# Optimization experiments

Measured on AMD Instinct MI355X. Metric: run time of the kernel, lower is better.

The kernel has to match this reference:

```python
import jax, jax.numpy as jnp
import numpy as np

N = 100000   # nodes
E = 800000   # edges
IN = 128     # input feature dim
H = 2        # heads
C = 64       # hidden_dim (per-head channels)
OUT = 40     # classes
L = 3        # num_layers
EPS = 1e-16  # matches torch_geometric.utils.softmax denominator eps


def setup_inputs() -> dict:
    key = jax.random.key(0)
    ks = jax.random.split(key, 4 * L + 6)
    inp = {}
    inp["x"] = jax.random.normal(ks[0], (N, IN), dtype=jnp.float32)
    inp["edge_index"] = jax.random.randint(ks[1], (2, E), 0, N, dtype=jnp.int32)
    dims = [IN] + [H * C] * (L - 1)
    ki = 2
    for l in range(L):
        d = dims[l]
        inp[f"W{l}"] = jax.random.normal(ks[ki], (H * C, d), dtype=jnp.float32) / np.float32(np.sqrt(d)); ki += 1
        inp[f"b{l}"] = jnp.zeros((H * C,), dtype=jnp.float32)
        inp[f"al{l}"] = jax.random.normal(ks[ki], (H, C), dtype=jnp.float32) * 0.1; ki += 1
        inp[f"ar{l}"] = jax.random.normal(ks[ki], (H, C), dtype=jnp.float32) * 0.1; ki += 1
    inp["Wp1"] = jax.random.normal(ks[ki], (C, H * C), dtype=jnp.float32) / np.float32(np.sqrt(H * C)); ki += 1
    inp["bp1"] = jnp.zeros((C,), dtype=jnp.float32)
    inp["Wp2"] = jax.random.normal(ks[ki], (OUT, C), dtype=jnp.float32) / np.float32(np.sqrt(C)); ki += 1
    inp["bp2"] = jnp.zeros((OUT,), dtype=jnp.float32)
    return inp


def _gat_layer(x, W, b, al, ar, src, dst):
    # lin_l == lin_r (shared weights in the original)
    h = (x @ W.T + b).reshape(-1, H, C)          # [N, H, C]
    alpha_l = al * h                              # source-side scores [N, H, C]
    alpha_r = ar * h                              # target-side scores [N, H, C]
    # per-edge raw attention logits; NOTE: original computes leaky_relu(alpha)
    # but then applies softmax to the RAW sum (faithful to source code).
    e = alpha_r[dst] + alpha_l[src]               # [E, H, C]
    m = jax.ops.segment_max(e, dst, num_segments=N)
    w = jnp.exp(e - m[dst])
    s = jax.ops.segment_sum(w, dst, num_segments=N)
    att = w / (s[dst] + EPS)                      # segment softmax per target node
    out = jax.ops.segment_sum(att * h[src], dst, num_segments=N)  # [N, H, C]
    return out.reshape(-1, H * C)


def reference(x, edge_index, W0, b0, al0, ar0, W1, b1, al1, ar1, W2, b2, al2, ar2,
              Wp1, bp1, Wp2, bp2):
    src, dst = edge_index[0], edge_index[1]
    layers = [(W0, b0, al0, ar0), (W1, b1, al1, ar1), (W2, b2, al2, ar2)]
    h = x
    for (W, b, al, ar) in layers:
        h = _gat_layer(h, W, b, al, ar, src, dst)
        h = jax.nn.relu(h)  # dropout p=0 -> identity
    h = h @ Wp1.T + bp1
    h = h @ Wp2.T + bp2
    return jax.nn.log_softmax(h, axis=1)
```

## Files before the change

kernel.cpp:

```cpp
#include <hip/hip_runtime.h>
#include <hip/hip_bf16.h>
#include <math.h>

#define NN 100000
#define EE 800000
#define DD 128
#define OUTC 40

constexpr int NBUCK = (NN + 511) >> 9;
constexpr int BCAP  = 6144;
constexpr int EB    = 8192;

typedef short bf16x8 __attribute__((ext_vector_type(8)));
typedef float f32x4 __attribute__((ext_vector_type(4)));

__device__ __forceinline__ ushort f2bf(float f) {
  unsigned u = __float_as_uint(f);
  u = (u + 0x7FFFu + ((u >> 16) & 1u)) >> 16;
  return (ushort)u;
}
__device__ __forceinline__ float bflo(unsigned u) { return __uint_as_float(u << 16); }
__device__ __forceinline__ float bfhi(unsigned u) { return __uint_as_float(u & 0xFFFF0000u); }

__device__ __forceinline__ int swz(int row, int kbyte) {
  return row * 256 + (kbyte ^ ((row & 7) << 4));
}

__global__ __launch_bounds__(256) void k_initcur(int* __restrict__ cursor0) {
  int b = threadIdx.x;
  if (b < NBUCK) cursor0[b] = b * BCAP;
}

__global__ __launch_bounds__(256) void k_binA(const int* __restrict__ src, const int* __restrict__ dst,
                                              int* __restrict__ cursor0, int2* __restrict__ binned, int e) {
  __shared__ int cnt[NBUCK], base[NBUCK], cnt2[NBUCK];
  int t = threadIdx.x;
  for (int b = t; b < NBUCK; b += 256) { cnt[b] = 0; cnt2[b] = 0; }
  __syncthreads();
  int e0 = blockIdx.x * EB;
#pragma unroll
  for (int p = 0; p < EB / 256; ++p) {
    int i = e0 + p * 256 + t;
    if (i < e) atomicAdd(&cnt[dst[i] >> 9], 1);
  }
  __syncthreads();
  for (int b = t; b < NBUCK; b += 256)
    if (cnt[b] > 0) base[b] = atomicAdd(&cursor0[b], cnt[b]);
  __syncthreads();
#pragma unroll
  for (int p = 0; p < EB / 256; ++p) {
    int i = e0 + p * 256 + t;
    if (i < e) {
      int d = dst[i];
      int bk = d >> 9;
      int pos = base[bk] + atomicAdd(&cnt2[bk], 1);
      binned[pos] = make_int2(src[i], d);
    }
  }
}

__global__ __launch_bounds__(256) void k_degB(const int* __restrict__ cursor0,
                                              const int2* __restrict__ binned,
                                              int* __restrict__ deg, int n) {
  __shared__ int cnt[512];
  int b = blockIdx.x, t = threadIdx.x;
  cnt[t] = 0; cnt[t + 256] = 0;
  __syncthreads();
  int node0 = b << 9;
  int beg = b * BCAP;
  int cend = cursor0[b];
  for (int i = beg + t; i < cend; i += 256)
    atomicAdd(&cnt[binned[i].y - node0], 1);
  __syncthreads();
  if (node0 + t < n) deg[node0 + t] = cnt[t];
  if (node0 + t + 256 < n) deg[node0 + t + 256] = cnt[t + 256];
}

__global__ __launch_bounds__(1024) void k_scan1(const int* __restrict__ deg, int* __restrict__ rp,
                                                int* __restrict__ bsum, int n) {
  __shared__ int s[1024];
  int t = threadIdx.x;
  int i = blockIdx.x * 1024 + t;
  s[t] = (i < n) ? deg[i] : 0;
  __syncthreads();
  for (int off = 1; off < 1024; off <<= 1) {
    int x = (t >= off) ? s[t - off] : 0;
    __syncthreads();
    s[t] += x;
    __syncthreads();
  }
  if (i < n) rp[i + 1] = s[t];
  if (t == 1023) bsum[blockIdx.x] = s[1023];
}

__global__ __launch_bounds__(128) void k_scan2(int* __restrict__ bsum, int nb) {
  __shared__ int s[128];
  int t = threadIdx.x;
  s[t] = (t < nb) ? bsum[t] : 0;
  __syncthreads();
  for (int off = 1; off < 128; off <<= 1) {
    int x = (t >= off) ? s[t - off] : 0;
    __syncthreads();
    s[t] += x;
    __syncthreads();
  }
  if (t < nb) bsum[t] = s[t];
}

__global__ void k_scan3(int* __restrict__ rp, const int* __restrict__ bsum, int n) {
  int i = blockIdx.x * 256 + threadIdx.x;
  if (i == 0) rp[0] = 0;
  if (i < n) {
    int blk = i >> 10;
    rp[i + 1] = rp[i + 1] + ((blk > 0) ? bsum[blk - 1] : 0);
  }
}

__global__ __launch_bounds__(256) void k_scatC(const int* __restrict__ cursor0,
                                               const int2* __restrict__ binned,
                                               const int* __restrict__ rp,
                                               int* __restrict__ col, int n) {
  __shared__ int cur[512];
  __shared__ int lrp[512];
  int b = blockIdx.x, t = threadIdx.x;
  cur[t] = 0; cur[t + 256] = 0;
  int node0 = b << 9;
  lrp[t] = (node0 + t < n) ? rp[node0 + t] : 0;
  lrp[t + 256] = (node0 + t + 256 < n) ? rp[node0 + t + 256] : 0;
  __syncthreads();
  int beg = b * BCAP;
  int cend = cursor0[b];
  for (int i = beg + t; i < cend; i += 256) {
    int2 p = binned[i];
    int d = p.y - node0;
    int pos = lrp[d] + atomicAdd(&cur[d], 1);
    col[pos] = p.x;
  }
}

template<bool INF32>
__global__ __launch_bounds__(256, 2) void k_mfma_gemm(const void* __restrict__ xin,
                                                      const float* __restrict__ W,
                                                      const float* __restrict__ bias,
                                                      ushort* __restrict__ outp, int n) {
  __shared__ __align__(16) char lds[65536];
  const int t = threadIdx.x;
  const int node0 = blockIdx.x * 128;

  if (INF32) {
#pragma unroll
    for (int p = 0; p < 16; ++p) {
      int F = p * 256 + t;
      int r = F >> 5, cchunk = F & 31;
      int node = node0 + r;
      float4 v = make_float4(0.f, 0.f, 0.f, 0.f);
      if (node < n) v = *(const float4*)((const float*)xin + (size_t)node * DD + cchunk * 4);
      ushort q[4] = {f2bf(v.x), f2bf(v.y), f2bf(v.z), f2bf(v.w)};
      *(unsigned long long*)(lds + swz(r, cchunk * 8)) = *(unsigned long long*)q;
    }
  } else {
#pragma unroll
    for (int p = 0; p < 8; ++p) {
      int F = p * 256 + t;
      int r = F >> 4, cchunk = F & 15;
      int node = node0 + r;
      uint4 v = make_uint4(0u, 0u, 0u, 0u);
      if (node < n) v = *(const uint4*)((const ushort*)xin + (size_t)node * DD + cchunk * 8);
      *(uint4*)(lds + swz(r, cchunk * 16)) = v;
    }
  }
  {
#pragma unroll
    for (int p = 0; p < 16; ++p) {
      int F = p * 256 + t;
      int r = F >> 5, cchunk = F & 31;
      float4 v = *(const float4*)(W + (size_t)r * DD + cchunk * 4);
      ushort q[4] = {f2bf(v.x), f2bf(v.y), f2bf(v.z), f2bf(v.w)};
      *(unsigned long long*)(lds + 32768 + swz(r, cchunk * 8)) = *(unsigned long long*)q;
    }
  }
  __syncthreads();

  const int lane = t & 63;
  const int l15 = lane & 15;
  const int lkb = (lane >> 4) * 16;
  const int wrow0 = (t >> 6) * 32;

  f32x4 acc[2][8];
#pragma unroll
  for (int j = 0; j < 8; ++j) {
    float bv = bias[j * 16 + l15];
    acc[0][j] = (f32x4){bv, bv, bv, bv};
    acc[1][j] = (f32x4){bv, bv, bv, bv};
  }

#pragma unroll
  for (int c = 0; c < 4; ++c) {
    bf16x8 a0 = *(const bf16x8*)(lds + swz(wrow0 + l15, c * 64 + lkb));
    bf16x8 a1 = *(const bf16x8*)(lds + swz(wrow0 + 16 + l15, c * 64 + lkb));
#pragma unroll
    for (int j = 0; j < 8; ++j) {
      bf16x8 b = *(const bf16x8*)(lds + 32768 + swz(j * 16 + l15, c * 64 + lkb));
      acc[0][j] = __builtin_amdgcn_mfma_f32_16x16x32_bf16(a0, b, acc[0][j], 0, 0, 0);
      acc[1][j] = __builtin_amdgcn_mfma_f32_16x16x32_bf16(a1, b, acc[1][j], 0, 0, 0);
    }
  }

  const int rbase = wrow0 + (lane >> 4) * 4;
#pragma unroll
  for (int i = 0; i < 2; ++i) {
#pragma unroll
    for (int r = 0; r < 4; ++r) {
      int node = node0 + rbase + i * 16 + r;
      if (node < n) {
#pragma unroll
        for (int j = 0; j < 8; ++j)
          outp[(size_t)node * DD + j * 16 + l15] = f2bf(acc[i][j][r]);
      }
    }
  }
}

__global__ __launch_bounds__(256) void k_gat_agg(const ushort* __restrict__ h, const int* __restrict__ rp,
                                                 const int* __restrict__ col, const float* __restrict__ al,
                                                 const float* __restrict__ ar, ushort* __restrict__ out, int n) {
  int node = blockIdx.x * 4 + (threadIdx.x >> 6);
  int lane = threadIdx.x & 63;
  if (node >= n) return;
  const unsigned* hu = (const unsigned*)h;
  float al0 = al[2 * lane], al1 = al[2 * lane + 1];
  unsigned ud = hu[(unsigned)(node * 64 + lane)];
  float base0 = ar[2 * lane] * bflo(ud);
  float base1 = ar[2 * lane + 1] * bfhi(ud);
  int beg = __builtin_amdgcn_readfirstlane(rp[node]);
  int end = __builtin_amdgcn_readfirstlane(rp[node + 1]);
  float num0 = 0.f, num1 = 0.f, den0 = 0.f, den1 = 0.f;
#define ACCUM(U) { \
    float h0 = bflo(U), h1 = bfhi(U); \
    float w0 = __expf(fmaf(al0, h0, base0)); \
    float w1 = __expf(fmaf(al1, h1, base1)); \
    den0 += w0; den1 += w1; \
    num0 = fmaf(w0, h0, num0); num1 = fmaf(w1, h1, num1); }
  int j = beg;
  for (; j + 8 <= end; j += 8) {
    int s0 = __builtin_amdgcn_readfirstlane(col[j]);
    int s1 = __builtin_amdgcn_readfirstlane(col[j + 1]);
    int s2 = __builtin_amdgcn_readfirstlane(col[j + 2]);
    int s3 = __builtin_amdgcn_readfirstlane(col[j + 3]);
    int s4 = __builtin_amdgcn_readfirstlane(col[j + 4]);
    int s5 = __builtin_amdgcn_readfirstlane(col[j + 5]);
    int s6 = __builtin_amdgcn_readfirstlane(col[j + 6]);
    int s7 = __builtin_amdgcn_readfirstlane(col[j + 7]);
    unsigned u0 = hu[(unsigned)(s0 * 64 + lane)];
    unsigned u1 = hu[(unsigned)(s1 * 64 + lane)];
    unsigned u2 = hu[(unsigned)(s2 * 64 + lane)];
    unsigned u3 = hu[(unsigned)(s3 * 64 + lane)];
    unsigned u4 = hu[(unsigned)(s4 * 64 + lane)];
    unsigned u5 = hu[(unsigned)(s5 * 64 + lane)];
    unsigned u6 = hu[(unsigned)(s6 * 64 + lane)];
    unsigned u7 = hu[(unsigned)(s7 * 64 + lane)];
    ACCUM(u0); ACCUM(u1); ACCUM(u2); ACCUM(u3);
    ACCUM(u4); ACCUM(u5); ACCUM(u6); ACCUM(u7);
  }
  for (; j + 4 <= end; j += 4) {
    int s0 = __builtin_amdgcn_readfirstlane(col[j]);
    int s1 = __builtin_amdgcn_readfirstlane(col[j + 1]);
    int s2 = __builtin_amdgcn_readfirstlane(col[j + 2]);
    int s3 = __builtin_amdgcn_readfirstlane(col[j + 3]);
    unsigned u0 = hu[(unsigned)(s0 * 64 + lane)];
    unsigned u1 = hu[(unsigned)(s1 * 64 + lane)];
    unsigned u2 = hu[(unsigned)(s2 * 64 + lane)];
    unsigned u3 = hu[(unsigned)(s3 * 64 + lane)];
    ACCUM(u0); ACCUM(u1); ACCUM(u2); ACCUM(u3);
  }
  for (; j + 2 <= end; j += 2) {
    int s0 = __builtin_amdgcn_readfirstlane(col[j]);
    int s1 = __builtin_amdgcn_readfirstlane(col[j + 1]);
    unsigned u0 = hu[(unsigned)(s0 * 64 + lane)];
    unsigned u1 = hu[(unsigned)(s1 * 64 + lane)];
    ACCUM(u0); ACCUM(u1);
  }
  for (; j < end; ++j) {
    int s = __builtin_amdgcn_readfirstlane(col[j]);
    unsigned u = hu[(unsigned)(s * 64 + lane)];
    ACCUM(u);
  }
#undef ACCUM
  float o0 = fmaxf(num0 / (den0 + 1e-16f), 0.f);
  float o1 = fmaxf(num1 / (den1 + 1e-16f), 0.f);
  ((unsigned*)out)[(unsigned)(node * 64 + lane)] = (unsigned)f2bf(o0) | ((unsigned)f2bf(o1) << 16);
}

__global__ __launch_bounds__(256, 2) void k_final_fused(const ushort* __restrict__ xin,
                                                        const float* __restrict__ W1,
                                                        const float* __restrict__ b1,
                                                        const float* __restrict__ Wp2,
                                                        const float* __restrict__ bp2,
                                                        float* __restrict__ out, int n) {
  __shared__ __align__(16) char lds[49152];
  const int t = threadIdx.x;
  const int node0 = blockIdx.x * 128;

#pragma unroll
  for (int p = 0; p < 8; ++p) {
    int F = p * 256 + t;
    int r = F >> 4, cchunk = F & 15;
    int node = node0 + r;
    uint4 v = make_uint4(0u, 0u, 0u, 0u);
    if (node < n) v = *(const uint4*)(xin + (size_t)node * DD + cchunk * 8);
    *(uint4*)(lds + swz(r, cchunk * 16)) = v;
  }
#pragma unroll
  for (int p = 0; p < 8; ++p) {
    int F = p * 256 + t;
    int r = F >> 5, cchunk = F & 31;
    float4 v = *(const float4*)(W1 + (size_t)r * DD + cchunk * 4);
    ushort q[4] = {f2bf(v.x), f2bf(v.y), f2bf(v.z), f2bf(v.w)};
    *(unsigned long long*)(lds + 32768 + swz(r, cchunk * 8)) = *(unsigned long long*)q;
  }
  __syncthreads();

  const int lane = t & 63;
  const int l15 = lane & 15;
  const int lkb = (lane >> 4) * 16;
  const int wrow0 = (t >> 6) * 32;

  f32x4 acc[2][4];
#pragma unroll
  for (int j = 0; j < 4; ++j) {
    float bv = b1[j * 16 + l15];
    acc[0][j] = (f32x4){bv, bv, bv, bv};
    acc[1][j] = (f32x4){bv, bv, bv, bv};
  }
#pragma unroll
  for (int c = 0; c < 4; ++c) {
    bf16x8 a0 = *(const bf16x8*)(lds + swz(wrow0 + l15, c * 64 + lkb));
    bf16x8 a1 = *(const bf16x8*)(lds + swz(wrow0 + 16 + l15, c * 64 + lkb));
#pragma unroll
    for (int j = 0; j < 4; ++j) {
      bf16x8 b = *(const bf16x8*)(lds + 32768 + swz(j * 16 + l15, c * 64 + lkb));
      acc[0][j] = __builtin_amdgcn_mfma_f32_16x16x32_bf16(a0, b, acc[0][j], 0, 0, 0);
      acc[1][j] = __builtin_amdgcn_mfma_f32_16x16x32_bf16(a1, b, acc[1][j], 0, 0, 0);
    }
  }
  __syncthreads();

  float* h1L = (float*)lds;
  float* wpL = (float*)(lds + 34816);
  const int rbase = wrow0 + (lane >> 4) * 4;
#pragma unroll
  for (int i = 0; i < 2; ++i)
#pragma unroll
    for (int r = 0; r < 4; ++r) {
      int row = rbase + i * 16 + r;
#pragma unroll
      for (int j = 0; j < 4; ++j)
        h1L[row * 68 + j * 16 + l15] = acc[i][j][r];
    }
#pragma unroll
  for (int p = 0; p < 10; ++p) {
    int f = p * 256 + t;
    int o = f >> 6, q = f & 63;
    wpL[o * 68 + q] = Wp2[f];
  }
  __syncthreads();

  if (t < 128) {
    int node = node0 + t;
    if (node < n) {
      float u[OUTC];
#pragma unroll
      for (int o = 0; o < OUTC; ++o) u[o] = bp2[o];
#pragma unroll
      for (int qc = 0; qc < 16; ++qc) {
        f32x4 hv = *(const f32x4*)&h1L[t * 68 + qc * 4];
#pragma unroll
        for (int o = 0; o < OUTC; ++o) {
          f32x4 w = *(const f32x4*)&wpL[o * 68 + qc * 4];
          u[o] = fmaf(hv[3], w[3], fmaf(hv[2], w[2], fmaf(hv[1], w[1], fmaf(hv[0], w[0], u[o]))));
        }
      }
      float m = u[0];
#pragma unroll
      for (int o = 1; o < OUTC; ++o) m = fmaxf(m, u[o]);
      float ssum = 0.f;
#pragma unroll
      for (int o = 0; o < OUTC; ++o) ssum += __expf(u[o] - m);
      float ls = __logf(ssum) + m;
      float* op = out + (size_t)node * OUTC;
#pragma unroll
      for (int o = 0; o < OUTC; o += 4)
        *(float4*)&op[o] = make_float4(u[o] - ls, u[o + 1] - ls, u[o + 2] - ls, u[o + 3] - ls);
    }
  }
}

extern "C" void kernel_launch(void* const* d_in, const int* in_sizes, int n_in,
                              void* d_out, int out_size, void* d_ws, size_t ws_size,
                              hipStream_t stream) {
  const float* x   = (const float*)d_in[0];
  const int*   ei  = (const int*)d_in[1];
  const float* W[3]  = {(const float*)d_in[2],  (const float*)d_in[6],  (const float*)d_in[10]};
  const float* B[3]  = {(const float*)d_in[3],  (const float*)d_in[7],  (const float*)d_in[11]};
  const float* AL[3] = {(const float*)d_in[4],  (const float*)d_in[8],  (const float*)d_in[12]};
  const float* AR[3] = {(const float*)d_in[5],  (const float*)d_in[9],  (const float*)d_in[13]};
  const float* Wp1 = (const float*)d_in[14];
  const float* bp1 = (const float*)d_in[15];
  const float* Wp2 = (const float*)d_in[16];
  const float* bp2 = (const float*)d_in[17];
  float* outp = (float*)d_out;

  const int n = NN, e = EE;
  const int* srcp = ei;
  const int* dstp = ei + e;

  char* ws = (char*)d_ws;
  size_t off = 0;
  auto alloc = [&](size_t bytes) { void* p = ws + off; off = (off + bytes + 255) & ~(size_t)255; return p; };
  ushort* bhA = (ushort*)alloc((size_t)n * DD * 2);
  ushort* bhB = (ushort*)alloc((size_t)n * DD * 2);
  int*   deg   = (int*)alloc((size_t)n * 4);
  int*   rp    = (int*)alloc((size_t)(n + 1) * 4);
  int*   bsum  = (int*)alloc(1024 * 4);
  int*   col   = (int*)alloc((size_t)e * 4);
  int*   cursor0 = (int*)alloc((size_t)NBUCK * 4);
  int2*  binned  = (int2*)alloc((size_t)NBUCK * BCAP * 8);
  (void)ws_size;

  k_initcur<<<1, 256, 0, stream>>>(cursor0);
  k_binA<<<(e + EB - 1) / EB, 256, 0, stream>>>(srcp, dstp, cursor0, binned, e);
  k_degB<<<NBUCK, 256, 0, stream>>>(cursor0, binned, deg, n);
  int nb = (n + 1023) / 1024;
  k_scan1<<<nb, 1024, 0, stream>>>(deg, rp, bsum, n);
  k_scan2<<<1, 128, 0, stream>>>(bsum, nb);
  k_scan3<<<(n + 255) / 256, 256, 0, stream>>>(rp, bsum, n);
  k_scatC<<<NBUCK, 256, 0, stream>>>(cursor0, binned, rp, col, n);

  const int gblocks = (n + 127) / 128;
  const int ablocks = (n + 3) / 4;
  k_mfma_gemm<true><<<gblocks, 256, 0, stream>>>(x, W[0], B[0], bhA, n);
  k_gat_agg<<<ablocks, 256, 0, stream>>>(bhA, rp, col, AL[0], AR[0], bhB, n);
  for (int l = 1; l < 3; ++l) {
    k_mfma_gemm<false><<<gblocks, 256, 0, stream>>>(bhB, W[l], B[l], bhA, n);
    k_gat_agg<<<ablocks, 256, 0, stream>>>(bhA, rp, col, AL[l], AR[l], bhB, n);
  }
  k_final_fused<<<gblocks, 256, 0, stream>>>(bhB, Wp1, bp1, Wp2, bp2, outp, n);
}
```

Measured before the change: 375.6 us.

## Use MFMA for final 64->40 projection and log-softmax, shrink binning edge block

The final classifier layer previously ran on only 128 of 256 threads, each doing a scalar fp32 64x40 dot product from LDS. It now stores the hidden activations and Wp2 as swizzled bf16 in LDS and computes the projection with bf16 MFMA across all four waves. Log-softmax is then done with cross-lane shuffles, with padded classes masked by -1e30. The binning kernel's edge block size also drops from 8192 to 2048 to launch more blocks. The cost is extra bf16 rounding in the last layer and more shared-memory atomic setup per block in binning.

Result: faster. 345.6 us (-8.0%).

```diff
diff --git a/kernel.cpp b/kernel.cpp
--- a/kernel.cpp
+++ b/kernel.cpp
@@ -9,7 +9,7 @@
 
 constexpr int NBUCK = (NN + 511) >> 9;
 constexpr int BCAP  = 6144;
-constexpr int EB    = 8192;
+constexpr int EB    = 2048;
 
 typedef short bf16x8 __attribute__((ext_vector_type(8)));
 typedef float f32x4 __attribute__((ext_vector_type(4)));
@@ -24,6 +24,9 @@
 
 __device__ __forceinline__ int swz(int row, int kbyte) {
   return row * 256 + (kbyte ^ ((row & 7) << 4));
+}
+__device__ __forceinline__ int swz128(int row, int kbyte) {
+  return row * 128 + (kbyte ^ ((row & 7) << 4));
 }
 
 __global__ __launch_bounds__(256) void k_initcur(int* __restrict__ cursor0) {
@@ -300,6 +303,11 @@
   __shared__ __align__(16) char lds[49152];
   const int t = threadIdx.x;
   const int node0 = blockIdx.x * 128;
+  const int lane = t & 63;
+  const int l15 = lane & 15;
+  const int lg = lane >> 4;
+  const int lkb = lg * 16;
+  const int wrow0 = (t >> 6) * 32;
 
 #pragma unroll
   for (int p = 0; p < 8; ++p) {
@@ -320,11 +328,6 @@
   }
   __syncthreads();
 
-  const int lane = t & 63;
-  const int l15 = lane & 15;
-  const int lkb = (lane >> 4) * 16;
-  const int wrow0 = (t >> 6) * 32;
-
   f32x4 acc[2][4];
 #pragma unroll
   for (int j = 0; j < 4; ++j) {
@@ -345,9 +348,9 @@
   }
   __syncthreads();
 
-  float* h1L = (float*)lds;
-  float* wpL = (float*)(lds + 34816);
-  const int rbase = wrow0 + (lane >> 4) * 4;
+  char* h1L = lds;
+  char* wpL = lds + 16384;
+  const int rbase = wrow0 + lg * 4;
 #pragma unroll
   for (int i = 0; i < 2; ++i)
 #pragma unroll
@@ -355,42 +358,58 @@
       int row = rbase + i * 16 + r;
 #pragma unroll
       for (int j = 0; j < 4; ++j)
-        h1L[row * 68 + j * 16 + l15] = acc[i][j][r];
-    }
-#pragma unroll
-  for (int p = 0; p < 10; ++p) {
-    int f = p * 256 + t;
-    int o = f >> 6, q = f & 63;
-    wpL[o * 68 + q] = Wp2[f];
-  }
-  __syncthreads();
-
-  if (t < 128) {
-    int node = node0 + t;
-    if (node < n) {
-      float u[OUTC];
-#pragma unroll
-      for (int o = 0; o < OUTC; ++o) u[o] = bp2[o];
-#pragma unroll
-      for (int qc = 0; qc < 16; ++qc) {
-        f32x4 hv = *(const f32x4*)&h1L[t * 68 + qc * 4];
-#pragma unroll
-        for (int o = 0; o < OUTC; ++o) {
-          f32x4 w = *(const f32x4*)&wpL[o * 68 + qc * 4];
-          u[o] = fmaf(hv[3], w[3], fmaf(hv[2], w[2], fmaf(hv[1], w[1], fmaf(hv[0], w[0], u[o]))));
-        }
+        *(ushort*)(h1L + swz128(row, (j * 16 + l15) * 2)) = f2bf(acc[i][j][r]);
+    }
+#pragma unroll
+  for (int p = 0; p < 3; ++p) {
+    int flat = p * 1024 + t * 4;
+    int row = flat >> 6, ch0 = flat & 63;
+    float4 v = make_float4(0.f, 0.f, 0.f, 0.f);
+    if (row < OUTC) v = *(const float4*)(Wp2 + row * 64 + ch0);
+    ushort q[4] = {f2bf(v.x), f2bf(v.y), f2bf(v.z), f2bf(v.w)};
+    *(unsigned long long*)(wpL + swz128(row, ch0 * 2)) = *(unsigned long long*)q;
+  }
+  __syncthreads();
+
+  f32x4 acc2[2][3];
+#pragma unroll
+  for (int j = 0; j < 3; ++j) {
+    int cls = j * 16 + l15;
+    float bv = (cls < OUTC) ? bp2[cls] : -1e30f;
+    acc2[0][j] = (f32x4){bv, bv, bv, bv};
+    acc2[1][j] = (f32x4){bv, bv, bv, bv};
+  }
+#pragma unroll
+  for (int c2 = 0; c2 < 2; ++c2) {
+    bf16x8 a0 = *(const bf16x8*)(h1L + swz128(wrow0 + l15, c2 * 64 + lkb));
+    bf16x8 a1 = *(const bf16x8*)(h1L + swz128(wrow0 + 16 + l15, c2 * 64 + lkb));
+#pragma unroll
+    for (int j = 0; j < 3; ++j) {
+      bf16x8 b = *(const bf16x8*)(wpL + swz128(j * 16 + l15, c2 * 64 + lkb));
+      acc2[0][j] = __builtin_amdgcn_mfma_f32_16x16x32_bf16(a0, b, acc2[0][j], 0, 0, 0);
+      acc2[1][j] = __builtin_amdgcn_mfma_f32_16x16x32_bf16(a1, b, acc2[1][j], 0, 0, 0);
+    }
+  }
+
+#pragma unroll
+  for (int i = 0; i < 2; ++i) {
+#pragma unroll
+    for (int r = 0; r < 4; ++r) {
+      float u0 = acc2[i][0][r], u1 = acc2[i][1][r], u2 = acc2[i][2][r];
+      float m = fmaxf(fmaxf(u0, u1), u2);
+#pragma unroll
+      for (int d = 1; d < 16; d <<= 1) m = fmaxf(m, __shfl_xor(m, d, 64));
+      float s = __expf(u0 - m) + __expf(u1 - m) + __expf(u2 - m);
+#pragma unroll
+      for (int d = 1; d < 16; d <<= 1) s += __shfl_xor(s, d, 64);
+      float ls = __logf(s) + m;
+      int node = node0 + rbase + i * 16 + r;
+      if (node < n) {
+        float* op = out + (size_t)node * OUTC;
+        op[l15] = u0 - ls;
+        op[16 + l15] = u1 - ls;
+        if (l15 < 8) op[32 + l15] = u2 - ls;
       }
-      float m = u[0];
-#pragma unroll
-      for (int o = 1; o < OUTC; ++o) m = fmaxf(m, u[o]);
-      float ssum = 0.f;
-#pragma unroll
-      for (int o = 0; o < OUTC; ++o) ssum += __expf(u[o] - m);
-      float ls = __logf(ssum) + m;
-      float* op = out + (size_t)node * OUTC;
-#pragma unroll
-      for (int o = 0; o < OUTC; o += 4)
-        *(float4*)&op[o] = make_float4(u[o] - ls, u[o + 1] - ls, u[o + 2] - ls, u[o + 3] - ls);
     }
   }
 }
```
